# Kernel optimization log

Hardware: AMD Instinct MI355X
Metric: run time of the kernel (lower is better)

The kernel has to match this reference:

```python
import jax, jax.numpy as jnp
import numpy as np

N_USERS = 100000
N_ITEMS = 50000
N_NODES = N_USERS + N_ITEMS
NNZ = 1600000          # user-item interactions
EMBED_DIM = 64
N_LAYERS = 3
NORM_EPS = 1e-12       # F.normalize eps
DEG_EPS = 1e-07        # degree eps from module


def _build_graph():
    rng = np.random.default_rng(0)
    u = rng.integers(0, N_USERS, NNZ)
    v = rng.integers(0, N_ITEMS, NNZ)
    # dedupe (row, col) pairs so COO has unique entries, matching (A>0) degree logic
    pair = np.unique(u.astype(np.int64) * N_ITEMS + v.astype(np.int64))
    u = (pair // N_ITEMS).astype(np.int32)
    v = (pair % N_ITEMS).astype(np.int32)
    rows = np.concatenate([u, v + N_USERS]).astype(np.int32)
    cols = np.concatenate([v + N_USERS, u]).astype(np.int32)
    deg = np.bincount(rows, minlength=N_NODES).astype(np.float32)
    dinv = np.power(deg + DEG_EPS, -0.5).astype(np.float32)
    vals = dinv[rows] * dinv[cols]
    return rows, cols, vals


def setup_inputs() -> dict:
    key = jax.random.key(0)
    rows, cols, vals = _build_graph()
    in_embs = jax.random.normal(key, (N_NODES, EMBED_DIM), dtype=jnp.float32)
    return {
        "in_embs": in_embs,
        "rows": jnp.asarray(rows),
        "cols": jnp.asarray(cols),
        "vals": jnp.asarray(vals),
    }


def reference(in_embs, rows, cols, vals):
    n = in_embs.shape[0]
    x = in_embs
    out = in_embs
    for i in range(N_LAYERS):
        # SpMM: A_norm @ x  via edge gather + segment_sum scatter
        msg = vals[:, None] * x[cols]                      # [E, d]
        x = jax.ops.segment_sum(msg, rows, num_segments=n)  # [n, d]
        # F.normalize(x, dim=-1)
        norm = jnp.linalg.norm(x, axis=-1, keepdims=True)
        x = x / jnp.maximum(norm, NORM_EPS)
        out = out + x / (i + 1)
    return out
```

## Files before the change

### kernel.cpp

```cpp
#include <hip/hip_runtime.h>
#include <hip/hip_bf16.h>


constexpr int N_USERS = 100000;
constexpr int N_ITEMS = 50000;
constexpr int N_NODES = N_USERS + N_ITEMS;
constexpr int D = 64;
constexpr int NBK  = 196;
constexpr int SLOT = 12288;
constexpr int EPB  = 16384;

__device__ inline unsigned f2bf(float f) {
    unsigned u = __float_as_uint(f);
    u += 0x7FFFu + ((u >> 16) & 1u);
    return u >> 16;
}
__device__ inline float bflo(unsigned u) { return __uint_as_float(u << 16); }
__device__ inline float bfhi(unsigned u) { return __uint_as_float(u & 0xFFFF0000u); }

__device__ inline int lower_bound(const int* __restrict__ a, int n, int key) {
    int lo = 0, hi = n;
    while (lo < hi) { int m = (lo + hi) >> 1; if (a[m] < key) lo = m + 1; else hi = m; }
    return lo;
}

__global__ __launch_bounds__(256) void rpu_kernel(
    const int* __restrict__ rows, int* __restrict__ rpu,
    float* __restrict__ dinv, int* __restrict__ bcur, int Eh)
{
    if (blockIdx.x == 0 && threadIdx.x < NBK) bcur[threadIdx.x] = threadIdx.x * SLOT;
    int i = blockIdx.x * 256 + threadIdx.x;
    if (i > N_USERS) return;
    int lo = lower_bound(rows, Eh, i);
    rpu[i] = lo;
    int lane = threadIdx.x & 63;
    int nxt = __shfl_down(lo, 1);
    if (lane == 63 || i >= N_USERS)
        nxt = (i < N_USERS) ? lower_bound(rows, Eh, i + 1) : lo;
    if (i < N_USERS)
        dinv[i] = rsqrtf((float)(nxt - lo) + 1e-7f);
}

__global__ __launch_bounds__(256) void bucket_scatter(
    const int* __restrict__ rows, const int* __restrict__ cols,
    int* __restrict__ bcur, int* __restrict__ staging, int Eh)
{
    __shared__ int hist[256];
    const int tid = threadIdx.x;
    const int base = blockIdx.x * EPB;
    const int nEdge = min(EPB, Eh - base);
    if (nEdge <= 0) return;

    hist[tid] = 0;
    __syncthreads();

    for (int s = 0; s < 16; ++s) {
        int o = s * 1024 + tid * 4;
        if (o + 3 < nEdge) {
            int4 c4 = *reinterpret_cast<const int4*>(cols + base + o);
            atomicAdd(&hist[(c4.x - N_USERS) >> 8], 1);
            atomicAdd(&hist[(c4.y - N_USERS) >> 8], 1);
            atomicAdd(&hist[(c4.z - N_USERS) >> 8], 1);
            atomicAdd(&hist[(c4.w - N_USERS) >> 8], 1);
        } else if (o < nEdge) {
            for (int k = o; k < nEdge; ++k)
                atomicAdd(&hist[(cols[base + k] - N_USERS) >> 8], 1);
        }
    }
    __syncthreads();

    if (tid < NBK) {
        int h = hist[tid];
        hist[tid] = (h > 0) ? atomicAdd(&bcur[tid], h) : 0;
    }
    __syncthreads();

    for (int s = 0; s < 16; ++s) {
        int o = s * 1024 + tid * 4;
        if (o + 3 < nEdge) {
            int4 c4 = *reinterpret_cast<const int4*>(cols + base + o);
            int4 u4 = *reinterpret_cast<const int4*>(rows + base + o);
            int v, p;
            v = c4.x - N_USERS; p = atomicAdd(&hist[v >> 8], 1);
            staging[p] = ((v & 255) << 24) | u4.x;
            v = c4.y - N_USERS; p = atomicAdd(&hist[v >> 8], 1);
            staging[p] = ((v & 255) << 24) | u4.y;
            v = c4.z - N_USERS; p = atomicAdd(&hist[v >> 8], 1);
            staging[p] = ((v & 255) << 24) | u4.z;
            v = c4.w - N_USERS; p = atomicAdd(&hist[v >> 8], 1);
            staging[p] = ((v & 255) << 24) | u4.w;
        } else if (o < nEdge) {
            for (int k = o; k < nEdge; ++k) {
                int v = cols[base + k] - N_USERS;
                int u = rows[base + k];
                int p = atomicAdd(&hist[v >> 8], 1);
                staging[p] = ((v & 255) << 24) | u;
            }
        }
    }
}

__global__ __launch_bounds__(256) void item_csr(
    const int* __restrict__ bcur, const int* __restrict__ staging,
    int* __restrict__ rpi, float* __restrict__ dinv, int* __restrict__ csr)
{
    __shared__ int hist[256];
    __shared__ int cur[256];
    __shared__ int wsum[4];
    __shared__ int s_cbase;
    const int b = blockIdx.x;
    const int tid = threadIdx.x, lane = tid & 63, w = tid >> 6;

    int tot = (tid < NBK) ? (bcur[tid] - tid * SLOT) : 0;
    int incl = tot;
    #pragma unroll
    for (int off = 1; off < 64; off <<= 1) {
        int s = __shfl_up(incl, off);
        if (lane >= off) incl += s;
    }
    if (lane == 63) wsum[w] = incl;
    __syncthreads();
    int woff = 0;
    #pragma unroll
    for (int k = 0; k < 4; ++k) woff += (k < w) ? wsum[k] : 0;
    int excl = woff + incl - tot;
    if (tid == b) s_cbase = excl;
    if (b == 0 && tid == NBK - 1) rpi[N_ITEMS] = excl + tot;
    __syncthreads();

    const int sbase = b * SLOT;
    const int n = bcur[b] - sbase;
    const int cbase = s_cbase;

    hist[tid] = 0;
    __syncthreads();
    for (int i = tid; i < n; i += 256)
        atomicAdd(&hist[((unsigned)staging[sbase + i]) >> 24], 1);
    __syncthreads();

    int h = hist[tid];
    int incl2 = h;
    #pragma unroll
    for (int off = 1; off < 64; off <<= 1) {
        int s = __shfl_up(incl2, off);
        if (lane >= off) incl2 += s;
    }
    if (lane == 63) wsum[w] = incl2;
    __syncthreads();
    int woff2 = 0;
    #pragma unroll
    for (int k = 0; k < 4; ++k) woff2 += (k < w) ? wsum[k] : 0;
    int excl2 = woff2 + incl2 - h;

    int gitem = b * 256 + tid;
    if (gitem < N_ITEMS) {
        rpi[gitem] = cbase + excl2;
        dinv[N_USERS + gitem] = rsqrtf((float)h + 1e-7f);
    }
    cur[tid] = cbase + excl2;
    __syncthreads();

    for (int i = tid; i < n; i += 256) {
        int e = staging[sbase + i];
        int p = atomicAdd(&cur[((unsigned)e) >> 24], 1);
        csr[p] = e & 0xFFFFFF;
    }
}

__global__ __launch_bounds__(256) void prep0(
    const float* __restrict__ init, const float* __restrict__ dinv,
    unsigned short* __restrict__ z)
{
    int i = blockIdx.x * 256 + threadIdx.x;
    if (i >= N_NODES * D / 4) return;
    int r = i >> 4;
    float dv = dinv[r];
    float4 x = reinterpret_cast<const float4*>(init)[i];
    unsigned lo0 = f2bf(x.x * dv), hi0 = f2bf(x.y * dv);
    unsigned lo1 = f2bf(x.z * dv), hi1 = f2bf(x.w * dv);
    uint2 o; o.x = lo0 | (hi0 << 16); o.y = lo1 | (hi1 << 16);
    reinterpret_cast<uint2*>(z)[i] = o;
}

#define ACC8(r) do { \
    a0 += bflo(r.x); a1 += bfhi(r.x); \
    a2 += bflo(r.y); a3 += bfhi(r.y); \
    a4 += bflo(r.z); a5 += bfhi(r.z); \
    a6 += bflo(r.w); a7 += bfhi(r.w); } while (0)

template<int LAST>
__global__ __launch_bounds__(256) void spmm8(
    const unsigned short* __restrict__ z,
    const int* __restrict__ rpu,
    const int* __restrict__ rpi,
    const int* __restrict__ cols_u,
    const int* __restrict__ csr_col_i,
    const float* __restrict__ dinv,
    unsigned short* __restrict__ zout,
    const unsigned short* z1,
    const unsigned short* z2,
    const float* __restrict__ init,
    float* __restrict__ out)
{
    const int tid = threadIdx.x;
    const int lane = tid & 63;
    const int g  = lane >> 3;
    const int sl = lane & 7;
    const int wave = tid >> 6;
    const int row = blockIdx.x * 32 + wave * 8 + g;
    if (row >= N_NODES) return;
    const int gb = g << 3;

    int beg, end;
    const int* clist;
    if (row < N_USERS) {
        beg = rpu[row]; end = rpu[row + 1]; clist = cols_u;
    } else {
        int v = row - N_USERS;
        beg = rpi[v]; end = rpi[v + 1]; clist = csr_col_i;
    }

    float a0=0.f,a1=0.f,a2=0.f,a3=0.f,a4=0.f,a5=0.f,a6=0.f,a7=0.f;
    const unsigned short* zs = z + (size_t)sl * 8;

    int j = beg;
    for (; j + 8 <= end; j += 8) {
        int c_l = clist[j + sl];
        int c0 = __shfl(c_l, gb + 0);
        int c1 = __shfl(c_l, gb + 1);
        int c2 = __shfl(c_l, gb + 2);
        int c3 = __shfl(c_l, gb + 3);
        int c4 = __shfl(c_l, gb + 4);
        int c5 = __shfl(c_l, gb + 5);
        int c6 = __shfl(c_l, gb + 6);
        int c7 = __shfl(c_l, gb + 7);
        uint4 r0 = *reinterpret_cast<const uint4*>(zs + (size_t)c0 * D);
        uint4 r1 = *reinterpret_cast<const uint4*>(zs + (size_t)c1 * D);
        uint4 r2 = *reinterpret_cast<const uint4*>(zs + (size_t)c2 * D);
        uint4 r3 = *reinterpret_cast<const uint4*>(zs + (size_t)c3 * D);
        uint4 r4 = *reinterpret_cast<const uint4*>(zs + (size_t)c4 * D);
        uint4 r5 = *reinterpret_cast<const uint4*>(zs + (size_t)c5 * D);
        uint4 r6 = *reinterpret_cast<const uint4*>(zs + (size_t)c6 * D);
        uint4 r7 = *reinterpret_cast<const uint4*>(zs + (size_t)c7 * D);
        ACC8(r0); ACC8(r1); ACC8(r2); ACC8(r3);
        ACC8(r4); ACC8(r5); ACC8(r6); ACC8(r7);
    }
    int rem = end - j;
    if (rem > 0) {
        int c_l = (j + sl < end) ? clist[j + sl] : 0;
        for (int k = 0; k < rem; ++k) {
            int c = __shfl(c_l, gb + k);
            uint4 r = *reinterpret_cast<const uint4*>(zs + (size_t)c * D);
            ACC8(r);
        }
    }

    float ss = a0*a0 + a1*a1 + a2*a2 + a3*a3 + a4*a4 + a5*a5 + a6*a6 + a7*a7;
    ss += __shfl_xor(ss, 1);
    ss += __shfl_xor(ss, 2);
    ss += __shfl_xor(ss, 4);
    float rinv = 1.0f / fmaxf(sqrtf(ss), 1e-12f);

    size_t idx = (size_t)row * D + (size_t)sl * 8;
    if (!LAST) {
        float s = rinv * dinv[row];
        uint4 zo;
        zo.x = f2bf(a0 * s) | (f2bf(a1 * s) << 16);
        zo.y = f2bf(a2 * s) | (f2bf(a3 * s) << 16);
        zo.z = f2bf(a4 * s) | (f2bf(a5 * s) << 16);
        zo.w = f2bf(a6 * s) | (f2bf(a7 * s) << 16);
        *reinterpret_cast<uint4*>(zout + idx) = zo;
    } else {
        float recip = 1.0f / dinv[row];
        float k1 = recip, k2 = 0.5f * recip, k3 = rinv * (1.0f / 3.0f);
        uint4 w1 = *reinterpret_cast<const uint4*>(z1 + idx);
        uint4 w2 = *reinterpret_cast<const uint4*>(z2 + idx);
        const float4* ip = reinterpret_cast<const float4*>(init + idx);
        float4 o0 = ip[0], o1 = ip[1];
        o0.x += bflo(w1.x) * k1 + bflo(w2.x) * k2 + a0 * k3;
        o0.y += bfhi(w1.x) * k1 + bfhi(w2.x) * k2 + a1 * k3;
        o0.z += bflo(w1.y) * k1 + bflo(w2.y) * k2 + a2 * k3;
        o0.w += bfhi(w1.y) * k1 + bfhi(w2.y) * k2 + a3 * k3;
        o1.x += bflo(w1.z) * k1 + bflo(w2.z) * k2 + a4 * k3;
        o1.y += bfhi(w1.z) * k1 + bfhi(w2.z) * k2 + a5 * k3;
        o1.z += bflo(w1.w) * k1 + bflo(w2.w) * k2 + a6 * k3;
        o1.w += bfhi(w1.w) * k1 + bfhi(w2.w) * k2 + a7 * k3;
        float4* op = reinterpret_cast<float4*>(out + idx);
        op[0] = o0; op[1] = o1;
    }
}

extern "C" void kernel_launch(void* const* d_in, const int* in_sizes, int n_in,
                              void* d_out, int out_size, void* d_ws, size_t ws_size,
                              hipStream_t stream) {
    const float* in_embs = (const float*)d_in[0];
    const int*   rows    = (const int*)d_in[1];
    const int*   cols    = (const int*)d_in[2];
    float* out = (float*)d_out;

    const int E  = in_sizes[1];
    const int Eh = E / 2;
    const size_t z_bytes = (size_t)N_NODES * D * sizeof(unsigned short);

    auto align256 = [](size_t x) { return (x + 255) & ~(size_t)255; };
    char* p = (char*)d_ws;
    unsigned short* zP = (unsigned short*)p; p += align256(z_bytes);
    unsigned short* zQ = (unsigned short*)p; p += align256(z_bytes);
    int*   csr_col_i = (int*)p;   p += align256((size_t)Eh * sizeof(int));
    int*   rpu       = (int*)p;   p += align256((size_t)(N_USERS + 1) * sizeof(int));
    int*   rpi       = (int*)p;   p += align256((size_t)(N_ITEMS + 1) * sizeof(int));
    float* dinv      = (float*)p; p += align256((size_t)N_NODES * sizeof(float));
    int*   bcur      = (int*)p;   p += align256(256 * sizeof(int));
    int*   staging   = (int*)zP;

    rpu_kernel<<<(N_USERS + 256) / 256, 256, 0, stream>>>(rows, rpu, dinv, bcur, Eh);
    bucket_scatter<<<(Eh + EPB - 1) / EPB, 256, 0, stream>>>(rows, cols, bcur, staging, Eh);
    item_csr<<<NBK, 256, 0, stream>>>(bcur, staging, rpi, dinv, csr_col_i);
    prep0<<<(N_NODES * D / 4 + 255) / 256, 256, 0, stream>>>(in_embs, dinv, zP);

    const int grid = (N_NODES + 31) / 32;
    spmm8<0><<<grid, 256, 0, stream>>>(zP, rpu, rpi, cols, csr_col_i, dinv,
                                       zQ, nullptr, nullptr, nullptr, nullptr);
    spmm8<0><<<grid, 256, 0, stream>>>(zQ, rpu, rpi, cols, csr_col_i, dinv,
                                       zP, nullptr, nullptr, nullptr, nullptr);
    spmm8<1><<<grid, 256, 0, stream>>>(zP, rpu, rpi, cols, csr_col_i, dinv,
                                       nullptr, zQ, zP, in_embs, out);
}
```

Baseline: 226.8 us.

## Assign one wavefront per row in SpMM with cross-lane reduction

The SpMM mapping moves from 8 lanes per row to a full 64-lane wavefront per row. Each 8-lane group gathers a different neighbour, and the partial sums are combined with xor shuffles. The first 64 column indices are loaded once into registers and broadcast by shuffle, and the epilogue loads and stores use nontemporal hints. The aim is more memory-level parallelism per row, at the cost of lane waste on low-degree rows (average degree is about 21) and extra shuffle-reduction overhead.

```diff
diff --git a/kernel.cpp b/kernel.cpp
--- a/kernel.cpp
+++ b/kernel.cpp
@@ -9,6 +9,9 @@
 constexpr int NBK  = 196;
 constexpr int SLOT = 12288;
 constexpr int EPB  = 16384;
+
+typedef unsigned int uint4v  __attribute__((ext_vector_type(4)));
+typedef float        float4v __attribute__((ext_vector_type(4)));
 
 __device__ inline unsigned f2bf(float f) {
     unsigned u = __float_as_uint(f);
@@ -189,7 +192,7 @@
     a6 += bflo(r.w); a7 += bfhi(r.w); } while (0)
 
 template<int LAST>
-__global__ __launch_bounds__(256) void spmm8(
+__global__ __launch_bounds__(256) void spmm_wave(
     const unsigned short* __restrict__ z,
     const int* __restrict__ rpu,
     const int* __restrict__ rpi,
@@ -202,14 +205,12 @@
     const float* __restrict__ init,
     float* __restrict__ out)
 {
-    const int tid = threadIdx.x;
-    const int lane = tid & 63;
-    const int g  = lane >> 3;
-    const int sl = lane & 7;
-    const int wave = tid >> 6;
-    const int row = blockIdx.x * 32 + wave * 8 + g;
+    const int lane = threadIdx.x & 63;
+    const int wv   = threadIdx.x >> 6;
+    const int row  = blockIdx.x * 4 + wv;
     if (row >= N_NODES) return;
-    const int gb = g << 3;
+    const int o = lane >> 3;
+    const int s = lane & 7;
 
     int beg, end;
     const int* clist;
@@ -219,40 +220,50 @@
         int v = row - N_USERS;
         beg = rpi[v]; end = rpi[v + 1]; clist = csr_col_i;
     }
+    const int deg = end - beg;
+
+    int c_l = (lane < deg) ? __builtin_nontemporal_load(clist + beg + lane) : 0;
 
     float a0=0.f,a1=0.f,a2=0.f,a3=0.f,a4=0.f,a5=0.f,a6=0.f,a7=0.f;
-    const unsigned short* zs = z + (size_t)sl * 8;
-
-    int j = beg;
-    for (; j + 8 <= end; j += 8) {
-        int c_l = clist[j + sl];
-        int c0 = __shfl(c_l, gb + 0);
-        int c1 = __shfl(c_l, gb + 1);
-        int c2 = __shfl(c_l, gb + 2);
-        int c3 = __shfl(c_l, gb + 3);
-        int c4 = __shfl(c_l, gb + 4);
-        int c5 = __shfl(c_l, gb + 5);
-        int c6 = __shfl(c_l, gb + 6);
-        int c7 = __shfl(c_l, gb + 7);
-        uint4 r0 = *reinterpret_cast<const uint4*>(zs + (size_t)c0 * D);
-        uint4 r1 = *reinterpret_cast<const uint4*>(zs + (size_t)c1 * D);
-        uint4 r2 = *reinterpret_cast<const uint4*>(zs + (size_t)c2 * D);
-        uint4 r3 = *reinterpret_cast<const uint4*>(zs + (size_t)c3 * D);
-        uint4 r4 = *reinterpret_cast<const uint4*>(zs + (size_t)c4 * D);
-        uint4 r5 = *reinterpret_cast<const uint4*>(zs + (size_t)c5 * D);
-        uint4 r6 = *reinterpret_cast<const uint4*>(zs + (size_t)c6 * D);
-        uint4 r7 = *reinterpret_cast<const uint4*>(zs + (size_t)c7 * D);
-        ACC8(r0); ACC8(r1); ACC8(r2); ACC8(r3);
-        ACC8(r4); ACC8(r5); ACC8(r6); ACC8(r7);
-    }
-    int rem = end - j;
+    const unsigned short* zs = z + (size_t)s * 8;
+
+    const int nreg = min(deg, 64);
+    int k = 0;
+    for (; k + 16 <= nreg; k += 16) {
+        int cA = __shfl(c_l, k + o);
+        int cB = __shfl(c_l, k + 8 + o);
+        uint4 rA = *reinterpret_cast<const uint4*>(zs + (size_t)cA * D);
+        uint4 rB = *reinterpret_cast<const uint4*>(zs + (size_t)cB * D);
+        ACC8(rA); ACC8(rB);
+    }
+    if (k + 8 <= nreg) {
+        int c = __shfl(c_l, k + o);
+        uint4 r = *reinterpret_cast<const uint4*>(zs + (size_t)c * D);
+        ACC8(r);
+        k += 8;
+    }
+    int rem = nreg - k;
     if (rem > 0) {
-        int c_l = (j + sl < end) ? clist[j + sl] : 0;
-        for (int k = 0; k < rem; ++k) {
-            int c = __shfl(c_l, gb + k);
+        int c = __shfl(c_l, k + o);
+        if (o < rem) {
             uint4 r = *reinterpret_cast<const uint4*>(zs + (size_t)c * D);
             ACC8(r);
         }
+    }
+    for (int j = beg + 64; j < end; j += 8) {
+        if (j + o < end) {
+            int c = __builtin_nontemporal_load(clist + j + o);
+            uint4 r = *reinterpret_cast<const uint4*>(zs + (size_t)c * D);
+            ACC8(r);
+        }
+    }
+
+    #pragma unroll
+    for (int off = 8; off <= 32; off <<= 1) {
+        a0 += __shfl_xor(a0, off); a1 += __shfl_xor(a1, off);
+        a2 += __shfl_xor(a2, off); a3 += __shfl_xor(a3, off);
+        a4 += __shfl_xor(a4, off); a5 += __shfl_xor(a5, off);
+        a6 += __shfl_xor(a6, off); a7 += __shfl_xor(a7, off);
     }
 
     float ss = a0*a0 + a1*a1 + a2*a2 + a3*a3 + a4*a4 + a5*a5 + a6*a6 + a7*a7;
@@ -261,22 +272,24 @@
     ss += __shfl_xor(ss, 4);
     float rinv = 1.0f / fmaxf(sqrtf(ss), 1e-12f);
 
-    size_t idx = (size_t)row * D + (size_t)sl * 8;
+    if (o != 0) return;
+    size_t idx = (size_t)row * D + (size_t)s * 8;
     if (!LAST) {
-        float s = rinv * dinv[row];
+        float sc = rinv * dinv[row];
         uint4 zo;
-        zo.x = f2bf(a0 * s) | (f2bf(a1 * s) << 16);
-        zo.y = f2bf(a2 * s) | (f2bf(a3 * s) << 16);
-        zo.z = f2bf(a4 * s) | (f2bf(a5 * s) << 16);
-        zo.w = f2bf(a6 * s) | (f2bf(a7 * s) << 16);
+        zo.x = f2bf(a0 * sc) | (f2bf(a1 * sc) << 16);
+        zo.y = f2bf(a2 * sc) | (f2bf(a3 * sc) << 16);
+        zo.z = f2bf(a4 * sc) | (f2bf(a5 * sc) << 16);
+        zo.w = f2bf(a6 * sc) | (f2bf(a7 * sc) << 16);
         *reinterpret_cast<uint4*>(zout + idx) = zo;
     } else {
         float recip = 1.0f / dinv[row];
         float k1 = recip, k2 = 0.5f * recip, k3 = rinv * (1.0f / 3.0f);
-        uint4 w1 = *reinterpret_cast<const uint4*>(z1 + idx);
-        uint4 w2 = *reinterpret_cast<const uint4*>(z2 + idx);
-        const float4* ip = reinterpret_cast<const float4*>(init + idx);
-        float4 o0 = ip[0], o1 = ip[1];
+        uint4v w1 = __builtin_nontemporal_load(reinterpret_cast<const uint4v*>(z1 + idx));
+        uint4v w2 = __builtin_nontemporal_load(reinterpret_cast<const uint4v*>(z2 + idx));
+        const float4v* ip = reinterpret_cast<const float4v*>(init + idx);
+        float4v o0 = __builtin_nontemporal_load(ip);
+        float4v o1 = __builtin_nontemporal_load(ip + 1);
         o0.x += bflo(w1.x) * k1 + bflo(w2.x) * k2 + a0 * k3;
         o0.y += bfhi(w1.x) * k1 + bfhi(w2.x) * k2 + a1 * k3;
         o0.z += bflo(w1.y) * k1 + bflo(w2.y) * k2 + a2 * k3;
@@ -285,8 +298,9 @@
         o1.y += bfhi(w1.z) * k1 + bfhi(w2.z) * k2 + a5 * k3;
         o1.z += bflo(w1.w) * k1 + bflo(w2.w) * k2 + a6 * k3;
         o1.w += bfhi(w1.w) * k1 + bfhi(w2.w) * k2 + a7 * k3;
-        float4* op = reinterpret_cast<float4*>(out + idx);
-        op[0] = o0; op[1] = o1;
+        float4v* op = reinterpret_cast<float4v*>(out + idx);
+        __builtin_nontemporal_store(o0, op);
+        __builtin_nontemporal_store(o1, op + 1);
     }
 }
 
@@ -318,11 +332,11 @@
     item_csr<<<NBK, 256, 0, stream>>>(bcur, staging, rpi, dinv, csr_col_i);
     prep0<<<(N_NODES * D / 4 + 255) / 256, 256, 0, stream>>>(in_embs, dinv, zP);
 
-    const int grid = (N_NODES + 31) / 32;
-    spmm8<0><<<grid, 256, 0, stream>>>(zP, rpu, rpi, cols, csr_col_i, dinv,
-                                       zQ, nullptr, nullptr, nullptr, nullptr);
-    spmm8<0><<<grid, 256, 0, stream>>>(zQ, rpu, rpi, cols, csr_col_i, dinv,
-                                       zP, nullptr, nullptr, nullptr, nullptr);
-    spmm8<1><<<grid, 256, 0, stream>>>(zP, rpu, rpi, cols, csr_col_i, dinv,
-                                       nullptr, zQ, zP, in_embs, out);
-}
+    const int grid = (N_NODES + 3) / 4;
+    spmm_wave<0><<<grid, 256, 0, stream>>>(zP, rpu, rpi, cols, csr_col_i, dinv,
+                                           zQ, nullptr, nullptr, nullptr, nullptr);
+    spmm_wave<0><<<grid, 256, 0, stream>>>(zQ, rpu, rpi, cols, csr_col_i, dinv,
+                                           zP, nullptr, nullptr, nullptr, nullptr);
+    spmm_wave<1><<<grid, 256, 0, stream>>>(zP, rpu, rpi, cols, csr_col_i, dinv,
+                                           nullptr, zQ, zP, in_embs, out);
+}
```

After: 292.1 us. +28.8%, slower.
